# Kernel optimization log

Hardware: AMD Instinct MI355X
Metric: run time of the kernel (lower is better)

The kernel has to match this reference:

```python
import jax, jax.numpy as jnp
import numpy as np
from itertools import product

C_IN, C_OUT = 32, 64
N_DOWN = 100000
CHILD = 4
N = N_DOWN * CHILD  # 400000 active voxels


def _encode(c):
    # pack nonnegative (x,y,z) voxel coords into a single int64 key
    c = c.astype(np.int64)
    return (c[:, 0] << 40) | (c[:, 1] << 20) | c[:, 2]


def _build_coords(rng):
    # N_DOWN unique parent voxels in [1,126]^3, each with exactly CHILD distinct children
    flat = rng.choice(126 ** 3, N_DOWN, replace=False)
    px = flat // (126 * 126) + 1
    py = (flat // 126) % 126 + 1
    pz = flat % 126 + 1
    parents = np.stack([px, py, pz], 1)  # [N_DOWN,3]
    child_off = rng.random((N_DOWN, 8)).argsort(1)[:, :CHILD]  # [N_DOWN,4] in 0..7
    bits = np.stack([child_off >> 2 & 1, child_off >> 1 & 1, child_off & 1], -1)  # [N_DOWN,4,3]
    children = (2 * parents[:, None, :] + bits).reshape(N, 3)
    kvec = child_off.reshape(N)  # kernel offset id of each child within its parent
    parent_of = np.repeat(np.arange(N_DOWN), CHILD)
    return children, kvec, parent_of


def _build_kmap3(children):
    # submanifold 3x3x3 neighbor map: km_in[k,i] = index j with coords[j] = coords[i] + off_k
    keys = _encode(children)
    order = np.argsort(keys)
    skeys = keys[order]
    offsets = list(product((-1, 0, 1), repeat=3))
    km_in = np.full((27, N), N, np.int32)
    km_out = np.full((27, N), N, np.int32)
    ar = np.arange(N, dtype=np.int32)
    for k, off in enumerate(offsets):
        nk = _encode(children + np.asarray(off))
        pos = np.clip(np.searchsorted(skeys, nk), 0, N - 1)
        found = skeys[pos] == nk
        km_in[k] = np.where(found, order[pos].astype(np.int32), N)
        km_out[k] = np.where(found, ar, N)
    return km_in, km_out


def _build_kmap_pool(kvec, parent_of):
    # kernel-2 stride-2 conv: each child feeds exactly one parent at offset kvec
    kp_in = np.full((8, N), N, np.int32)
    kp_out = np.full((8, N), N_DOWN, np.int32)
    for k in range(8):
        idx = np.nonzero(kvec == k)[0]
        kp_in[k, :len(idx)] = idx
        kp_out[k, :len(idx)] = parent_of[idx]
    return kp_in, kp_out


def setup_inputs() -> dict:
    rng = np.random.default_rng(0)
    children, kvec, parent_of = _build_coords(rng)
    km_in, km_out = _build_kmap3(children)
    kp_in, kp_out = _build_kmap_pool(kvec, parent_of)

    key = jax.random.key(0)
    ks = jax.random.split(key, 10)
    f32 = jnp.float32
    return {
        'x': jax.random.normal(ks[0], (N, C_IN), f32),
        'W1': jax.random.normal(ks[1], (27, C_IN, C_OUT), f32) * 0.05,
        'bn1_s': jax.random.uniform(ks[2], (C_OUT,), f32, 0.5, 1.5),
        'bn1_b': jax.random.normal(ks[3], (C_OUT,), f32) * 0.1,
        'W2': jax.random.normal(ks[4], (27, C_OUT, C_OUT), f32) * 0.05,
        'bn2_s': jax.random.uniform(ks[5], (C_OUT,), f32, 0.5, 1.5),
        'bn2_b': jax.random.normal(ks[6], (C_OUT,), f32) * 0.1,
        'Wp': jax.random.normal(ks[7], (8, C_OUT, C_OUT), f32) * 0.05,
        'bnp_s': jax.random.uniform(ks[8], (C_OUT,), f32, 0.5, 1.5),
        'bnp_b': jax.random.normal(ks[9], (C_OUT,), f32) * 0.1,
        'km_in': jnp.asarray(km_in),
        'km_out': jnp.asarray(km_out),
        'kp_in': jnp.asarray(kp_in),
        'kp_out': jnp.asarray(kp_out),
        'n_down': N_DOWN,
    }


def _sparse_conv(x, W, iidx, oidx, n_out):
    # gather -> per-offset matmul -> scatter-add; invalid pairs point at zero row / dump row
    xp = jnp.concatenate([x, jnp.zeros((1, x.shape[1]), x.dtype)], 0)
    def body(acc, a):
        Wk, ii, oi = a
        return acc.at[oi].add(xp[ii] @ Wk), None
    acc0 = jnp.zeros((n_out + 1, W.shape[2]), x.dtype)
    acc, _ = jax.lax.scan(body, acc0, (W, iidx, oidx))
    return acc[:n_out]


def _bn_relu(h, s, b):
    return jax.nn.relu(h * s + b)


def reference(x, W1, bn1_s, bn1_b, W2, bn2_s, bn2_b, Wp, bnp_s, bnp_b,
              km_in, km_out, kp_in, kp_out, n_down):
    n = x.shape[0]
    h = _bn_relu(_sparse_conv(x, W1, km_in, km_out, n), bn1_s, bn1_b)
    down = _bn_relu(_sparse_conv(h, W2, km_in, km_out, n), bn2_s, bn2_b)
    p = _bn_relu(_sparse_conv(down, Wp, kp_in, kp_out, n_down), bnp_s, bnp_b)
    return (down, p)
```

## Files before the change

kernel.cpp:

```cpp
#include <hip/hip_runtime.h>


#define NV 400000
#define ND 100000

typedef __attribute__((ext_vector_type(8))) short  bf16x8;
typedef __attribute__((ext_vector_type(4))) float  f32x4;

__device__ __forceinline__ unsigned short f2b(float f) {
    unsigned int u = __builtin_bit_cast(unsigned int, f);
    u += 0x7fffu + ((u >> 16) & 1u);
    return (unsigned short)(u >> 16);
}

__global__ __launch_bounds__(256) void cvt_bf16_k(
    const float* __restrict__ in, unsigned short* __restrict__ out, int n)
{
    int t = (blockIdx.x * 256 + threadIdx.x) * 4;
    if (t >= n) return;
    float4 f = *(const float4*)(in + t);
    ushort4 u;
    u.x = f2b(f.x); u.y = f2b(f.y); u.z = f2b(f.z); u.w = f2b(f.w);
    *(ushort4*)(out + t) = u;
}

__global__ __launch_bounds__(256) void pack_w_k(
    const float* __restrict__ W, unsigned short* __restrict__ out, int nk, int ci)
{
    int t = blockIdx.x * 256 + threadIdx.x;
    int steps = ci >> 5;
    if (t >= nk * steps * 4 * 64) return;
    int lane = t & 63;
    int nt   = (t >> 6) & 3;
    int rest = t >> 8;
    int s    = rest % steps;
    int k    = rest / steps;
    int col = lane & 15, quad = lane >> 4;
    int co = nt * 16 + col;
    unsigned short v[8];
#pragma unroll
    for (int j = 0; j < 8; ++j) {
        int cidx = s * 32 + quad * 8 + j;
        v[j] = f2b(W[((size_t)k * ci + cidx) * 64 + co]);
    }
    bf16x8 frag;
#pragma unroll
    for (int j = 0; j < 8; ++j) frag[j] = (short)v[j];
    *(bf16x8*)(out + (size_t)t * 8) = frag;
}

__global__ __launch_bounds__(256) void ck_init_k(int* __restrict__ ck)
{
    int t = blockIdx.x * 256 + threadIdx.x;
    if (t < ND * 8) ck[t] = NV;
}
__global__ __launch_bounds__(256) void ck_scatter_k(
    const int* __restrict__ kp_in, const int* __restrict__ kp_out,
    int* __restrict__ ck)
{
    int t = blockIdx.x * 256 + threadIdx.x;
    if (t >= 8 * NV) return;
    int j = kp_in[t];
    if (j == NV) return;
    int k = t / NV;
    ck[kp_out[t] * 8 + k] = j;
}

template <int CI, int NK, bool OUT_BF16>
__global__ __launch_bounds__(256) void conv_mfma(
    const unsigned short* __restrict__ xin,
    const unsigned short* __restrict__ Wp,
    const int* __restrict__ km,
    const float* __restrict__ bns, const float* __restrict__ bnb,
    void* __restrict__ outp)
{
    constexpr int STEPS = CI / 32;
    const int lane = threadIdx.x & 63;
    const int wave = threadIdx.x >> 6;
    const int col = lane & 15, quad = lane >> 4;
    const int wbase = (blockIdx.x * 4 + wave) * 64;

    f32x4 acc[4][4];
#pragma unroll
    for (int mt = 0; mt < 4; ++mt)
#pragma unroll
        for (int nt = 0; nt < 4; ++nt) acc[mt][nt] = (f32x4)0.f;

    for (int k = 0; k < NK; ++k) {
        const int* __restrict__ kmr = km + (size_t)k * NV;
        int j[4];
#pragma unroll
        for (int mt = 0; mt < 4; ++mt) {
            int row = wbase + mt * 16 + col;
            j[mt] = kmr[row < NV ? row : NV - 1];
        }
#pragma unroll
        for (int s = 0; s < STEPS; ++s) {
            bf16x8 a[4];
#pragma unroll
            for (int mt = 0; mt < 4; ++mt)
                a[mt] = *(const bf16x8*)(xin + (size_t)j[mt] * CI + s * 32 + quad * 8);
            const unsigned short* bp = Wp + ((((size_t)k * STEPS + s) * 4) * 64 + lane) * 8;
#pragma unroll
            for (int nt = 0; nt < 4; ++nt) {
                bf16x8 b = *(const bf16x8*)(bp + (size_t)nt * 64 * 8);
#pragma unroll
                for (int mt = 0; mt < 4; ++mt)
                    acc[mt][nt] = __builtin_amdgcn_mfma_f32_16x16x32_bf16(
                        a[mt], b, acc[mt][nt], 0, 0, 0);
            }
        }
    }

#pragma unroll
    for (int nt = 0; nt < 4; ++nt) {
        const int n = nt * 16 + col;
        const float sc = bns[n], bi = bnb[n];
#pragma unroll
        for (int mt = 0; mt < 4; ++mt)
#pragma unroll
            for (int r = 0; r < 4; ++r) {
                int row = wbase + mt * 16 + quad * 4 + r;
                if (row < NV) {
                    float v = fmaxf(fmaf(acc[mt][nt][r], sc, bi), 0.f);
                    if (OUT_BF16)
                        ((unsigned short*)outp)[(size_t)row * 64 + n] = f2b(v);
                    else
                        ((float*)outp)[(size_t)row * 64 + n] = v;
                }
            }
    }
}

__global__ __launch_bounds__(256) void pool_mfma(
    const float* __restrict__ down,
    const float* __restrict__ zrow,
    const unsigned short* __restrict__ Wp,
    const int* __restrict__ ck,
    const float* __restrict__ bns, const float* __restrict__ bnb,
    float* __restrict__ pout)
{
    const int lane = threadIdx.x & 63;
    const int wave = threadIdx.x >> 6;
    const int col = lane & 15, quad = lane >> 4;
    const int wbase = (blockIdx.x * 4 + wave) * 64;

    f32x4 acc[4][4];
#pragma unroll
    for (int mt = 0; mt < 4; ++mt)
#pragma unroll
        for (int nt = 0; nt < 4; ++nt) acc[mt][nt] = (f32x4)0.f;

    for (int kk = 0; kk < 8; ++kk) {
        int j[4];
#pragma unroll
        for (int mt = 0; mt < 4; ++mt) {
            int row = wbase + mt * 16 + col;
            j[mt] = ck[(size_t)(row < ND ? row : ND - 1) * 8 + kk];
        }
#pragma unroll
        for (int s = 0; s < 2; ++s) {
            bf16x8 a[4];
#pragma unroll
            for (int mt = 0; mt < 4; ++mt) {
                const float* ap = (j[mt] == NV ? zrow : down + (size_t)j[mt] * 64)
                                  + s * 32 + quad * 8;
                float4 f0 = *(const float4*)ap;
                float4 f1 = *(const float4*)(ap + 4);
                bf16x8 av;
                av[0] = (short)f2b(f0.x); av[1] = (short)f2b(f0.y);
                av[2] = (short)f2b(f0.z); av[3] = (short)f2b(f0.w);
                av[4] = (short)f2b(f1.x); av[5] = (short)f2b(f1.y);
                av[6] = (short)f2b(f1.z); av[7] = (short)f2b(f1.w);
                a[mt] = av;
            }
            const unsigned short* bp = Wp + ((((size_t)kk * 2 + s) * 4) * 64 + lane) * 8;
#pragma unroll
            for (int nt = 0; nt < 4; ++nt) {
                bf16x8 b = *(const bf16x8*)(bp + (size_t)nt * 64 * 8);
#pragma unroll
                for (int mt = 0; mt < 4; ++mt)
                    acc[mt][nt] = __builtin_amdgcn_mfma_f32_16x16x32_bf16(
                        a[mt], b, acc[mt][nt], 0, 0, 0);
            }
        }
    }

#pragma unroll
    for (int nt = 0; nt < 4; ++nt) {
        const int n = nt * 16 + col;
        const float sc = bns[n], bi = bnb[n];
#pragma unroll
        for (int mt = 0; mt < 4; ++mt)
#pragma unroll
            for (int r = 0; r < 4; ++r) {
                int row = wbase + mt * 16 + quad * 4 + r;
                if (row < ND) {
                    float v = fmaxf(fmaf(acc[mt][nt][r], sc, bi), 0.f);
                    pout[(size_t)row * 64 + n] = v;
                }
            }
    }
}

extern "C" void kernel_launch(void* const* d_in, const int* in_sizes, int n_in,
                              void* d_out, int out_size, void* d_ws, size_t ws_size,
                              hipStream_t stream)
{
    const float* x    = (const float*)d_in[0];
    const float* W1   = (const float*)d_in[1];
    const float* bn1s = (const float*)d_in[2];
    const float* bn1b = (const float*)d_in[3];
    const float* W2   = (const float*)d_in[4];
    const float* bn2s = (const float*)d_in[5];
    const float* bn2b = (const float*)d_in[6];
    const float* Wp   = (const float*)d_in[7];
    const float* bnps = (const float*)d_in[8];
    const float* bnpb = (const float*)d_in[9];
    const int* km_in  = (const int*)d_in[10];
    const int* kp_in  = (const int*)d_in[12];
    const int* kp_out = (const int*)d_in[13];

    float* down = (float*)d_out;
    float* pout = (float*)d_out + (size_t)NV * 64;

    char* ws = (char*)d_ws;
    unsigned short* x_bf  = (unsigned short*)ws;  ws += (size_t)(NV + 1) * 32 * 2;
    unsigned short* h_bf  = (unsigned short*)ws;  ws += (size_t)(NV + 1) * 64 * 2;
    int*            ck    = (int*)ws;             ws += (size_t)ND * 8 * 4;
    unsigned short* W1p   = (unsigned short*)ws;  ws += (size_t)27 * 32 * 64 * 2;
    unsigned short* W2p   = (unsigned short*)ws;  ws += (size_t)27 * 64 * 64 * 2;
    unsigned short* Wpp   = (unsigned short*)ws;  ws += (size_t)8 * 64 * 64 * 2;
    float*          zrow  = (float*)ws;

    hipMemsetAsync(x_bf + (size_t)NV * 32, 0, 32 * 2, stream);
    hipMemsetAsync(h_bf + (size_t)NV * 64, 0, 64 * 2, stream);
    hipMemsetAsync(zrow, 0, 64 * 4, stream);

    cvt_bf16_k<<<(NV * 32 / 4 + 255) / 256, 256, 0, stream>>>(x, x_bf, NV * 32);
    pack_w_k<<<(27 * 1 * 4 * 64 + 255) / 256, 256, 0, stream>>>(W1, W1p, 27, 32);
    pack_w_k<<<(27 * 2 * 4 * 64 + 255) / 256, 256, 0, stream>>>(W2, W2p, 27, 64);
    pack_w_k<<<(8  * 2 * 4 * 64 + 255) / 256, 256, 0, stream>>>(Wp, Wpp, 8, 64);
    ck_init_k<<<(ND * 8 + 255) / 256, 256, 0, stream>>>(ck);
    ck_scatter_k<<<(8 * NV + 255) / 256, 256, 0, stream>>>(kp_in, kp_out, ck);

    const int cgrid = (NV + 255) / 256;
    conv_mfma<32, 27, true ><<<cgrid, 256, 0, stream>>>(x_bf, W1p, km_in, bn1s, bn1b, h_bf);
    conv_mfma<64, 27, false><<<cgrid, 256, 0, stream>>>(h_bf, W2p, km_in, bn2s, bn2b, down);
    pool_mfma<<<(ND + 255) / 256, 256, 0, stream>>>(down, zrow, Wpp, ck, bnps, bnpb, pout);
}
```

Baseline: 606.6 us.

## Software-pipeline gathers in sparse conv and reuse it for bf16 pooling

The conv kernel now prefetches neighbor indices two offsets ahead and gathered input rows one offset ahead, so global-load latency overlaps the MFMA work of the current offset. The second conv also writes a bf16 copy of its output, which lets the pooling stage reuse the same templated conv kernel on bf16 inputs with a transposed (k-major) child map. This replaces the separate fp32-gather pooling kernel that converted to bf16 inside the loop. Index loads and fp32 output stores use nontemporal hints. The costs are extra registers for the prefetch buffers and an extra bf16 write of the down tensor.

```diff
diff --git a/kernel.cpp b/kernel.cpp
--- a/kernel.cpp
+++ b/kernel.cpp
@@ -63,16 +63,16 @@
     int j = kp_in[t];
     if (j == NV) return;
     int k = t / NV;
-    ck[kp_out[t] * 8 + k] = j;
-}
-
-template <int CI, int NK, bool OUT_BF16>
+    ck[(size_t)k * ND + kp_out[t]] = j;
+}
+
+template <int CI, int NK, int MODE, int NR>
 __global__ __launch_bounds__(256) void conv_mfma(
     const unsigned short* __restrict__ xin,
     const unsigned short* __restrict__ Wp,
     const int* __restrict__ km,
     const float* __restrict__ bns, const float* __restrict__ bnb,
-    void* __restrict__ outp)
+    float* __restrict__ outf, unsigned short* __restrict__ outb)
 {
     constexpr int STEPS = CI / 32;
     const int lane = threadIdx.x & 63;
@@ -80,35 +80,84 @@
     const int col = lane & 15, quad = lane >> 4;
     const int wbase = (blockIdx.x * 4 + wave) * 64;
 
+    int rowm[4];
+#pragma unroll
+    for (int mt = 0; mt < 4; ++mt) {
+        int r = wbase + mt * 16 + col;
+        rowm[mt] = r < NR ? r : NR - 1;
+    }
+
     f32x4 acc[4][4];
 #pragma unroll
     for (int mt = 0; mt < 4; ++mt)
 #pragma unroll
         for (int nt = 0; nt < 4; ++nt) acc[mt][nt] = (f32x4)0.f;
 
+    int j1[4];
+    bf16x8 aC0[4], aC1[4];
+    {
+        int jt[4];
+#pragma unroll
+        for (int mt = 0; mt < 4; ++mt)
+            jt[mt] = __builtin_nontemporal_load(km + rowm[mt]);
+#pragma unroll
+        for (int mt = 0; mt < 4; ++mt)
+            j1[mt] = __builtin_nontemporal_load(km + (size_t)NR + rowm[mt]);
+#pragma unroll
+        for (int mt = 0; mt < 4; ++mt)
+            aC0[mt] = *(const bf16x8*)(xin + (size_t)jt[mt] * CI + quad * 8);
+        if constexpr (STEPS == 2) {
+#pragma unroll
+            for (int mt = 0; mt < 4; ++mt)
+                aC1[mt] = *(const bf16x8*)(xin + (size_t)jt[mt] * CI + 32 + quad * 8);
+        }
+    }
+
+#pragma unroll 2
     for (int k = 0; k < NK; ++k) {
-        const int* __restrict__ kmr = km + (size_t)k * NV;
-        int j[4];
-#pragma unroll
-        for (int mt = 0; mt < 4; ++mt) {
-            int row = wbase + mt * 16 + col;
-            j[mt] = kmr[row < NV ? row : NV - 1];
-        }
-#pragma unroll
-        for (int s = 0; s < STEPS; ++s) {
-            bf16x8 a[4];
+        const int kk2 = (k + 2 < NK) ? k + 2 : NK - 1;
+        int j2[4];
+#pragma unroll
+        for (int mt = 0; mt < 4; ++mt)
+            j2[mt] = __builtin_nontemporal_load(km + (size_t)kk2 * NR + rowm[mt]);
+
+        const unsigned short* bp = Wp + (((size_t)(k * STEPS) * 4) * 64 + lane) * 8;
+
+#pragma unroll
+        for (int nt = 0; nt < 4; ++nt) {
+            bf16x8 b = *(const bf16x8*)(bp + (size_t)nt * 512);
 #pragma unroll
             for (int mt = 0; mt < 4; ++mt)
-                a[mt] = *(const bf16x8*)(xin + (size_t)j[mt] * CI + s * 32 + quad * 8);
-            const unsigned short* bp = Wp + ((((size_t)k * STEPS + s) * 4) * 64 + lane) * 8;
+                acc[mt][nt] = __builtin_amdgcn_mfma_f32_16x16x32_bf16(
+                    aC0[mt], b, acc[mt][nt], 0, 0, 0);
+        }
+
+        bf16x8 aN0[4], aN1[4];
+#pragma unroll
+        for (int mt = 0; mt < 4; ++mt)
+            aN0[mt] = *(const bf16x8*)(xin + (size_t)j1[mt] * CI + quad * 8);
+        if constexpr (STEPS == 2) {
+#pragma unroll
+            for (int mt = 0; mt < 4; ++mt)
+                aN1[mt] = *(const bf16x8*)(xin + (size_t)j1[mt] * CI + 32 + quad * 8);
+        }
+
+        if constexpr (STEPS == 2) {
 #pragma unroll
             for (int nt = 0; nt < 4; ++nt) {
-                bf16x8 b = *(const bf16x8*)(bp + (size_t)nt * 64 * 8);
+                bf16x8 b = *(const bf16x8*)(bp + 2048 + (size_t)nt * 512);
 #pragma unroll
                 for (int mt = 0; mt < 4; ++mt)
                     acc[mt][nt] = __builtin_amdgcn_mfma_f32_16x16x32_bf16(
-                        a[mt], b, acc[mt][nt], 0, 0, 0);
+                        aC1[mt], b, acc[mt][nt], 0, 0, 0);
             }
+        }
+
+#pragma unroll
+        for (int mt = 0; mt < 4; ++mt) {
+            aC0[mt] = aN0[mt];
+            if constexpr (STEPS == 2) aC1[mt] = aN1[mt];
+            j1[mt] = j2[mt];
         }
     }
 
@@ -121,83 +170,16 @@
 #pragma unroll
             for (int r = 0; r < 4; ++r) {
                 int row = wbase + mt * 16 + quad * 4 + r;
-                if (row < NV) {
+                if (row < NR) {
                     float v = fmaxf(fmaf(acc[mt][nt][r], sc, bi), 0.f);
-                    if (OUT_BF16)
-                        ((unsigned short*)outp)[(size_t)row * 64 + n] = f2b(v);
-                    else
-                        ((float*)outp)[(size_t)row * 64 + n] = v;
-                }
-            }
-    }
-}
-
-__global__ __launch_bounds__(256) void pool_mfma(
-    const float* __restrict__ down,
-    const float* __restrict__ zrow,
-    const unsigned short* __restrict__ Wp,
-    const int* __restrict__ ck,
-    const float* __restrict__ bns, const float* __restrict__ bnb,
-    float* __restrict__ pout)
-{
-    const int lane = threadIdx.x & 63;
-    const int wave = threadIdx.x >> 6;
-    const int col = lane & 15, quad = lane >> 4;
-    const int wbase = (blockIdx.x * 4 + wave) * 64;
-
-    f32x4 acc[4][4];
-#pragma unroll
-    for (int mt = 0; mt < 4; ++mt)
-#pragma unroll
-        for (int nt = 0; nt < 4; ++nt) acc[mt][nt] = (f32x4)0.f;
-
-    for (int kk = 0; kk < 8; ++kk) {
-        int j[4];
-#pragma unroll
-        for (int mt = 0; mt < 4; ++mt) {
-            int row = wbase + mt * 16 + col;
-            j[mt] = ck[(size_t)(row < ND ? row : ND - 1) * 8 + kk];
-        }
-#pragma unroll
-        for (int s = 0; s < 2; ++s) {
-            bf16x8 a[4];
-#pragma unroll
-            for (int mt = 0; mt < 4; ++mt) {
-                const float* ap = (j[mt] == NV ? zrow : down + (size_t)j[mt] * 64)
-                                  + s * 32 + quad * 8;
-                float4 f0 = *(const float4*)ap;
-                float4 f1 = *(const float4*)(ap + 4);
-                bf16x8 av;
-                av[0] = (short)f2b(f0.x); av[1] = (short)f2b(f0.y);
-                av[2] = (short)f2b(f0.z); av[3] = (short)f2b(f0.w);
-                av[4] = (short)f2b(f1.x); av[5] = (short)f2b(f1.y);
-                av[6] = (short)f2b(f1.z); av[7] = (short)f2b(f1.w);
-                a[mt] = av;
-            }
-            const unsigned short* bp = Wp + ((((size_t)kk * 2 + s) * 4) * 64 + lane) * 8;
-#pragma unroll
-            for (int nt = 0; nt < 4; ++nt) {
-                bf16x8 b = *(const bf16x8*)(bp + (size_t)nt * 64 * 8);
-#pragma unroll
-                for (int mt = 0; mt < 4; ++mt)
-                    acc[mt][nt] = __builtin_amdgcn_mfma_f32_16x16x32_bf16(
-                        a[mt], b, acc[mt][nt], 0, 0, 0);
-            }
-        }
-    }
-
-#pragma unroll
-    for (int nt = 0; nt < 4; ++nt) {
-        const int n = nt * 16 + col;
-        const float sc = bns[n], bi = bnb[n];
-#pragma unroll
-        for (int mt = 0; mt < 4; ++mt)
-#pragma unroll
-            for (int r = 0; r < 4; ++r) {
-                int row = wbase + mt * 16 + quad * 4 + r;
-                if (row < ND) {
-                    float v = fmaxf(fmaf(acc[mt][nt][r], sc, bi), 0.f);
-                    pout[(size_t)row * 64 + n] = v;
+                    if constexpr (MODE == 0) {
+                        __builtin_nontemporal_store(v, &outf[(size_t)row * 64 + n]);
+                    } else if constexpr (MODE == 1) {
+                        outb[(size_t)row * 64 + n] = f2b(v);
+                    } else {
+                        __builtin_nontemporal_store(v, &outf[(size_t)row * 64 + n]);
+                        outb[(size_t)row * 64 + n] = f2b(v);
+                    }
                 }
             }
     }
@@ -227,15 +209,15 @@
     char* ws = (char*)d_ws;
     unsigned short* x_bf  = (unsigned short*)ws;  ws += (size_t)(NV + 1) * 32 * 2;
     unsigned short* h_bf  = (unsigned short*)ws;  ws += (size_t)(NV + 1) * 64 * 2;
-    int*            ck    = (int*)ws;             ws += (size_t)ND * 8 * 4;
+    unsigned short* d_bf  = (unsigned short*)ws;  ws += (size_t)(NV + 1) * 64 * 2;
+    int*            ck    = (int*)ws;             ws += (size_t)8 * ND * 4;
     unsigned short* W1p   = (unsigned short*)ws;  ws += (size_t)27 * 32 * 64 * 2;
     unsigned short* W2p   = (unsigned short*)ws;  ws += (size_t)27 * 64 * 64 * 2;
-    unsigned short* Wpp   = (unsigned short*)ws;  ws += (size_t)8 * 64 * 64 * 2;
-    float*          zrow  = (float*)ws;
+    unsigned short* Wpp   = (unsigned short*)ws;
 
     hipMemsetAsync(x_bf + (size_t)NV * 32, 0, 32 * 2, stream);
     hipMemsetAsync(h_bf + (size_t)NV * 64, 0, 64 * 2, stream);
-    hipMemsetAsync(zrow, 0, 64 * 4, stream);
+    hipMemsetAsync(d_bf + (size_t)NV * 64, 0, 64 * 2, stream);
 
     cvt_bf16_k<<<(NV * 32 / 4 + 255) / 256, 256, 0, stream>>>(x, x_bf, NV * 32);
     pack_w_k<<<(27 * 1 * 4 * 64 + 255) / 256, 256, 0, stream>>>(W1, W1p, 27, 32);
@@ -245,7 +227,10 @@
     ck_scatter_k<<<(8 * NV + 255) / 256, 256, 0, stream>>>(kp_in, kp_out, ck);
 
     const int cgrid = (NV + 255) / 256;
-    conv_mfma<32, 27, true ><<<cgrid, 256, 0, stream>>>(x_bf, W1p, km_in, bn1s, bn1b, h_bf);
-    conv_mfma<64, 27, false><<<cgrid, 256, 0, stream>>>(h_bf, W2p, km_in, bn2s, bn2b, down);
-    pool_mfma<<<(ND + 255) / 256, 256, 0, stream>>>(down, zrow, Wpp, ck, bnps, bnpb, pout);
-}
+    conv_mfma<32, 27, 1, NV><<<cgrid, 256, 0, stream>>>(
+        x_bf, W1p, km_in, bn1s, bn1b, nullptr, h_bf);
+    conv_mfma<64, 27, 2, NV><<<cgrid, 256, 0, stream>>>(
+        h_bf, W2p, km_in, bn2s, bn2b, down, d_bf);
+    conv_mfma<64, 8, 0, ND><<<(ND + 255) / 256, 256, 0, stream>>>(
+        d_bf, Wpp, ck, bnps, bnpb, pout, nullptr);
+}
```

Measured after the change: 736.0 us. +21.3%, slower.
